# Performance work log

Hardware: AMD Instinct MI355X
Metric: run time of the kernel (lower is better)

The kernel has to match this reference:

```python
import jax, jax.numpy as jnp
import numpy as np

DWT_SCALE = 0.5   # per-tap Haar analysis scale (2D factor = 0.25)
IDWT_SCALE = 1.0  # per-tap Haar synthesis scale (exact inverse of 0.5 analysis)
CONV_PAD = 1      # (kernel_size - 1) // 2 for k = 3


def haar_dwt(x, s):
    # x: [B, C, H, W] -> [B, 4C, H/2, W/2], subband-major: [LL | LH | HL | HH]
    a = x[..., 0::2, 0::2]
    b = x[..., 0::2, 1::2]
    c = x[..., 1::2, 0::2]
    d = x[..., 1::2, 1::2]
    s2 = s * s
    ll = s2 * (a + b + c + d)
    lh = s2 * (a + b - c - d)
    hl = s2 * (a - b + c - d)
    hh = s2 * (a - b - c + d)
    return jnp.concatenate([ll, lh, hl, hh], axis=1)


def haar_idwt(y, t):
    # y: [B, 4C, H2, W2] -> [B, C, 2*H2, 2*W2]; exact inverse of haar_dwt when t*s == 0.5 per tap? (t=1, s=0.5 here)
    B, C4, H2, W2 = y.shape
    C = C4 // 4
    ll, lh, hl, hh = jnp.split(y, 4, axis=1)
    t2 = t * t
    a = t2 * (ll + lh + hl + hh)
    b = t2 * (ll + lh - hl - hh)
    c = t2 * (ll - lh + hl - hh)
    d = t2 * (ll - lh - hl + hh)
    top = jnp.stack([a, b], axis=-1).reshape(B, C, H2, 2 * W2)
    bot = jnp.stack([c, d], axis=-1).reshape(B, C, H2, 2 * W2)
    return jnp.stack([top, bot], axis=-2).reshape(B, C, 2 * H2, 2 * W2)


def conv2d(x, w, stride, pad):
    return jax.lax.conv_general_dilated(
        x, w, (stride, stride), [(pad, pad), (pad, pad)],
        dimension_numbers=('NCHW', 'OIHW', 'NCHW'))


def setup_inputs() -> dict:
    key = jax.random.key(0)
    ks = jax.random.split(key, 5)
    B, C, H, W, K, L = 4, 64, 192, 192, 3, 3
    x = jax.random.normal(ks[0], (B, C, H, W), dtype=jnp.float32)
    # kaiming_uniform_ with a=2.236: bound = sqrt(6 / ((1 + a^2) * fan_in))
    fan_in = 4 * C * K * K
    bound = float(np.sqrt(6.0 / ((1.0 + 2.236 ** 2) * fan_in)))
    inp = {'x': x}
    for i in range(L):
        inp[f'w{i}'] = jax.random.uniform(ks[1 + i], (4 * C, 4 * C, K, K), jnp.float32, -bound, bound)
    inp['bias'] = jnp.zeros((C,), jnp.float32)
    return inp


def reference(x, w0, w1, w2, bias):
    H, W = x.shape[-2:]
    weights = [w0, w1, w2]
    L = len(weights)
    pad_factor = 2 ** L
    pad_h = (-H) % pad_factor
    pad_w = (-W) % pad_factor
    xp = x
    if pad_h > 0 or pad_w > 0:
        xp = jnp.pad(x, ((0, 0), (0, 0), (0, pad_h), (0, pad_w)), mode='reflect')
    # decompose: DWT -> dense conv over stacked subbands; recurse on the conv'd LL band
    curr = xp
    highs = []
    for w in weights:
        d = haar_dwt(curr, DWT_SCALE)          # [B, 4C, H/2, W/2]
        y = conv2d(d, w, 1, CONV_PAD)          # [B, 4C_out, H/2, W/2]
        c_out = w.shape[0] // 4
        curr = y[:, :c_out]                    # LL -> next level
        highs.append(y[:, c_out:])             # LH, HL, HH kept for reconstruction
    # reconstruct bottom-up
    ll = curr
    for h in reversed(highs):
        ll = haar_idwt(jnp.concatenate([ll, h], axis=1), IDWT_SCALE)
    out = ll[..., :H, :W] + bias[None, :, None, None]
    return out
```

## Files before the change

### kernel.cpp

```cpp
#include <hip/hip_runtime.h>
#include <hip/hip_bf16.h>
#include <cstddef>


typedef __attribute__((ext_vector_type(8))) short short8;
typedef __attribute__((ext_vector_type(4))) float f32x4;
typedef __attribute__((ext_vector_type(4))) unsigned short u16x4;

static __device__ __forceinline__ unsigned short f2bf(float f) {
    __hip_bfloat16 h = __float2bfloat16(f);
    return *reinterpret_cast<unsigned short*>(&h);
}
static __device__ __forceinline__ float bf2f(unsigned short u) {
    return __uint_as_float(((unsigned int)u) << 16);
}

static __device__ __forceinline__ void gload_lds16(const short* g, short* l) {
    __builtin_amdgcn_global_load_lds(
        (const __attribute__((address_space(1))) void*)g,
        (__attribute__((address_space(3))) void*)l, 16, 0, 0);
}

__global__ __launch_bounds__(256) void mega_prep_kernel(
    const float* __restrict__ x,
    const float* __restrict__ wa, const float* __restrict__ wb,
    const float* __restrict__ wc,
    unsigned short* __restrict__ ta, unsigned short* __restrict__ tb,
    unsigned short* __restrict__ tc,
    unsigned short* __restrict__ p0, unsigned short* __restrict__ p1,
    unsigned short* __restrict__ p2)
{
    __shared__ float lds[4 * 64 * 17];
    const int bx = blockIdx.x;
    const int tid = threadIdx.x;
    if (bx < 864) {
        const int sel = bx / 288;
        const float* w = (sel == 0) ? wa : (sel == 1) ? wb : wc;
        unsigned short* wT = (sel == 0) ? ta : (sel == 1) ? tb : tc;
        int idx = (bx - sel * 288) * 256 + tid;
        int co = idx & 255;
        int g = (idx >> 8) & 3;
        int kb = (idx >> 10) & 7;
        int tap = idx >> 13;
        int cin0 = kb * 32 + g * 8;
        unsigned short tmp[8];
#pragma unroll
        for (int e = 0; e < 8; ++e)
            tmp[e] = f2bf(w[((size_t)co * 256 + cin0 + e) * 9 + tap]);
        *(short8*)(wT + (size_t)idx * 8) = *(const short8*)tmp;
        return;
    }
    if (bx < 1206) {
        constexpr int N0 = 49664, N1 = 25088, N2 = 12800;
        int idx = (bx - 864) * 256 + tid;
        unsigned short* base; int HP, WP, rel;
        if (idx < N0)           { base = p0; HP = 98; WP = 98; rel = idx; }
        else if (idx < N0 + N1) { base = p1; HP = 50; WP = 50; rel = idx - N0; }
        else                    { base = p2; HP = 26; WP = 26; rel = idx - N0 - N1; }
        int nb = 64 * WP + (HP - 2) * 64;
        int b = rel / nb, r = rel % nb;
        int row, kg, px;
        if (r < 64 * WP) {
            int rowSel = r / (32 * WP), rr = r % (32 * WP);
            kg = rr / WP; px = rr % WP; row = rowSel ? (HP - 1) : 0;
        } else {
            int r2 = r - 64 * WP;
            row = 1 + (r2 >> 6);
            int r3 = r2 & 63;
            kg = r3 >> 1; px = (r3 & 1) ? (WP - 1) : 0;
        }
        size_t o = (((size_t)(b * HP + row) * 32 + kg) * WP + px) * 8;
        short8 z = {};
        *(short8*)(base + o) = z;
        return;
    }
    const int bx2 = bx - 1206;
    const int j0 = (bx2 % 6) * 16;
    const int i  = (bx2 / 6) % 96;
    const int b  = bx2 / 576;
    const int j = tid & 15;
    const int c4 = tid >> 4;
#pragma unroll
    for (int it = 0; it < 4; ++it) {
        int c = c4 + it * 16;
        const float* p = x + ((size_t)(b * 64 + c) * 192 + 2 * i) * 192 + 2 * (j0 + j);
        float2 top = *(const float2*)p;
        float2 bot = *(const float2*)(p + 192);
        float a = top.x, bb = top.y, cc = bot.x, dd = bot.y;
        const float s2 = 0.25f;
        lds[(0 * 64 + c) * 17 + j] = s2 * (a + bb + cc + dd);
        lds[(1 * 64 + c) * 17 + j] = s2 * (a + bb - cc - dd);
        lds[(2 * 64 + c) * 17 + j] = s2 * (a - bb + cc - dd);
        lds[(3 * 64 + c) * 17 + j] = s2 * (a - bb - cc + dd);
    }
    __syncthreads();
#pragma unroll
    for (int it = 0; it < 2; ++it) {
        int idx = it * 256 + tid;
        int jj = idx & 15;
        int g = (idx >> 4) & 3;
        int kb = idx >> 6;
        int sub = kb >> 1;
        int c0 = (kb & 1) * 32 + g * 8;
        unsigned short tmp[8];
#pragma unroll
        for (int e = 0; e < 8; ++e)
            tmp[e] = f2bf(lds[(sub * 64 + c0 + e) * 17 + jj]);
        size_t o = ((((size_t)(b * 98 + 1 + i) * 8 + kb) * 4 + g) * 98 + 1 + j0 + jj) * 8;
        *(short8*)(p0 + o) = *(const short8*)tmp;
    }
}

template <int H2, int JB>
__global__ __launch_bounds__(256) void dwt_mid_kernel(
    const unsigned short* __restrict__ in, unsigned short* __restrict__ Xp)
{
    constexpr int W2 = H2, Wi = 2 * W2, WPn = W2 + 2, HPn = H2 + 2;
    constexpr int LS = JB + 1;
    __shared__ float lds[4 * 64 * LS];
    const int j0 = blockIdx.x * JB;
    const int i = blockIdx.y;
    const int b = blockIdx.z;
    const int tid = threadIdx.x;
    const int c = tid & 63;
    const int jq = tid >> 6;
#pragma unroll
    for (int it = 0; it < JB / 4; ++it) {
        int jl = jq + it * 4;
        int j = j0 + jl;
        const unsigned short* p = in + ((size_t)(b * 2 * H2 + 2 * i) * Wi + 2 * j) * 256 + c;
        float a  = bf2f(p[0]);
        float bb = bf2f(p[256]);
        float cc = bf2f(p[(size_t)Wi * 256]);
        float dd = bf2f(p[(size_t)Wi * 256 + 256]);
        const float s2 = 0.25f;
        lds[(0 * 64 + c) * LS + jl] = s2 * (a + bb + cc + dd);
        lds[(1 * 64 + c) * LS + jl] = s2 * (a + bb - cc - dd);
        lds[(2 * 64 + c) * LS + jl] = s2 * (a - bb + cc - dd);
        lds[(3 * 64 + c) * LS + jl] = s2 * (a - bb - cc + dd);
    }
    __syncthreads();
    constexpr int CH = 8 * 4 * JB;
#pragma unroll
    for (int it = 0; it < (CH + 255) / 256; ++it) {
        int idx = it * 256 + tid;
        if (idx < CH) {
            int jj = idx % JB;
            int g = (idx / JB) & 3;
            int kb = idx / (JB * 4);
            int sub = kb >> 1;
            int c0 = (kb & 1) * 32 + g * 8;
            unsigned short tmp[8];
#pragma unroll
            for (int e = 0; e < 8; ++e)
                tmp[e] = f2bf(lds[(sub * 64 + c0 + e) * LS + jj]);
            size_t o = ((((size_t)(b * HPn + 1 + i) * 8 + kb) * 4 + g) * WPn + 1 + j0 + jj) * 8;
            *(short8*)(Xp + o) = *(const short8*)tmp;
        }
    }
}

template <int HP, int WP, int PR, int PC, int XCHUNK>
__global__ __launch_bounds__(128) void conv_reg_kernel(
    const short* __restrict__ Xp, const short* __restrict__ Wt,
    unsigned short* __restrict__ Y)
{
    constexpr int WN = 2;
    constexpr int NPX = PR * PC;
    constexpr int MFR = 4;
    constexpr int NFR = NPX / (16 * WN);
    constexpr int RPF = 16 / PC;
    constexpr int BROWS = (NFR - 1) * RPF + 3;
    constexpr int H = HP - 2, W = WP - 2;
    constexpr int rowT = H / PR, colT = W / PC;
    constexpr int PH = PR + 2, PW = PC + 2;
    constexpr int RAW = PH * PW;
    constexpr int SLOTG = (RAW + 63) & ~63;
    constexpr int TI = 4 * SLOTG / 64;
    constexpr int TIW = TI / WN;
    constexpr size_t S_r = (size_t)256 * WP;
    constexpr size_t S_kb = (size_t)32 * WP;
    constexpr size_t S_g = (size_t)8 * WP;

    __shared__ __align__(16) short bufA[4 * SLOTG * 8];
    __shared__ __align__(16) short bufB[4 * SLOTG * 8];

    int bid = blockIdx.x;
    if (XCHUNK > 0) bid = (bid & 7) * XCHUNK + (bid >> 3);
    const int tx = bid % colT; bid /= colT;
    const int ty = bid % rowT; bid /= rowT;
    const int b = bid;
    const int gy0 = ty * PR;
    const int gx0 = tx * PC;
    const int cb = blockIdx.y * 64;

    const int lane = threadIdx.x & 63;
    const int wn = threadIdx.x >> 6;
    const int n15 = lane & 15, gq = lane >> 4;

    const size_t bBase = (size_t)(b * HP + gy0) * S_r + (size_t)gx0 * 8;

    size_t sSrc[TIW]; int sDst[TIW];
#pragma unroll
    for (int ti = 0; ti < TIW; ++ti) {
        int t = wn * TIW + ti;
        int d = t * 64 + lane;
        int g = d / SLOTG;
        int p = d - g * SLOTG;
        int prow = p / PW, pcol = p - prow * PW;
        sDst[ti] = d * 8;
        sSrc[ti] = (p < RAW)
            ? bBase + (size_t)prow * S_r + (size_t)g * S_g + (size_t)pcol * 8
            : bBase;
    }

    const short* aBase = Wt + (size_t)gq * 2048 + (size_t)(cb + n15) * 8;
    const int rB = wn * (PR / WN) + n15 / PC;
    const int cB = n15 % PC;
    const int bSlot = gq * SLOTG + rB * PW + cB;

    f32x4 acc[MFR][NFR] = {};
    short8 a[3][MFR];

    auto stage = [&](int kbv, short* dBuf) {
#pragma unroll
        for (int ti = 0; ti < TIW; ++ti)
            gload_lds16(Xp + sSrc[ti] + (size_t)kbv * S_kb, dBuf + sDst[ti]);
    };
    auto ldA = [&](int tap, int kbv, int m) -> short8 {
        return *(const short8*)(aBase + (size_t)tap * 65536
                                + (size_t)kbv * 8192 + m * 128);
    };

    stage(0, bufA);
#pragma unroll
    for (int s = 0; s < 3; ++s)
#pragma unroll
        for (int m = 0; m < MFR; ++m)
            a[s][m] = ldA(s, 0, m);
    asm volatile("s_waitcnt vmcnt(0)" ::: "memory");
    __builtin_amdgcn_sched_barrier(0);
    __builtin_amdgcn_s_barrier();

    auto kbBody = [&](int kb, const short* cur, short* nxt) {
        const int kbn = (kb < 7) ? kb + 1 : 7;
        stage(kbn, nxt);
        __builtin_amdgcn_sched_barrier(0);
        short8 Br[BROWS][3];
#pragma unroll
        for (int r = 0; r < BROWS; ++r)
#pragma unroll
            for (int kx = 0; kx < 3; ++kx)
                Br[r][kx] = *(const short8*)(cur + (bSlot + r * PW + kx) * 8);
#pragma unroll
        for (int s = 0; s < 9; ++s) {
            const int ky = s / 3, kx = s - 3 * (s / 3);
            const int rs = s % 3;
            __builtin_amdgcn_s_setprio(1);
#pragma unroll
            for (int m = 0; m < MFR; ++m)
#pragma unroll
                for (int n = 0; n < NFR; ++n)
                    acc[m][n] = __builtin_amdgcn_mfma_f32_16x16x32_bf16(
                        a[rs][m], Br[n * RPF + ky][kx], acc[m][n], 0, 0, 0);
            __builtin_amdgcn_s_setprio(0);
            const int ft = s + 3;
            const int ftap = (ft < 9) ? ft : ft - 9;
            const int fkb = (ft < 9) ? kb : kbn;
#pragma unroll
            for (int m = 0; m < MFR; ++m)
                a[rs][m] = ldA(ftap, fkb, m);
        }
        __builtin_amdgcn_sched_barrier(0);
        asm volatile("s_waitcnt vmcnt(36)" ::: "memory");
        __builtin_amdgcn_sched_barrier(0);
        __builtin_amdgcn_s_barrier();
    };

#pragma unroll 1
    for (int u = 0; u < 4; ++u) {
        kbBody(2 * u, bufA, bufB);
        kbBody(2 * u + 1, bufB, bufA);
    }
    asm volatile("s_waitcnt vmcnt(0)" ::: "memory");

#pragma unroll
    for (int m = 0; m < MFR; ++m)
#pragma unroll
        for (int n = 0; n < NFR; ++n) {
            int cout = cb + m * 16 + gq * 4;
            int row = wn * (PR / WN) + n * RPF + n15 / PC;
            int col = n15 % PC;
            unsigned short* op = Y + ((size_t)(b * H + gy0 + row) * W + gx0 + col) * 256 + cout;
            u16x4 sv;
#pragma unroll
            for (int q = 0; q < 4; ++q) sv[q] = f2bf(acc[m][n][q]);
            *(u16x4*)op = sv;
        }
}

__global__ __launch_bounds__(256) void idwt_fused_kernel(
    const unsigned short* __restrict__ y2, const unsigned short* __restrict__ y1,
    const unsigned short* __restrict__ y0h,
    const float* __restrict__ bias, float* __restrict__ out)
{
    __shared__ float lds[16 * 324];
    const int tt = blockIdx.x;
    const int tyi = tt / 12, txi = tt % 12;
    const int y0 = tyi * 8, x0 = txi * 8;
    const int cg = blockIdx.y;
    const int b = blockIdx.z;
    const int tid = threadIdx.x;

#pragma unroll
    for (int rep = 0; rep < 4; ++rep) {
        int idx = rep * 256 + tid;
        int c16 = idx & 15;
        int px = idx >> 4;
        int pi = px >> 3, pj = px & 7;
        int c = cg * 16 + c16;
        int pi96 = y0 + pi, pj96 = x0 + pj;
        int pi48 = pi96 >> 1, pj48 = pj96 >> 1;
        int pi24 = pi48 >> 1, pj24 = pj48 >> 1;
        const unsigned short* h2 = y2 + ((size_t)(b * 24 + pi24) * 24 + pj24) * 256;
        float l2   = bf2f(h2[c]);
        float l2lh = bf2f(h2[64 + c]);
        float l2hl = bf2f(h2[128 + c]);
        float l2hh = bf2f(h2[192 + c]);
        float s1 = 1.f - 2.f * (pi48 & 1), t1 = 1.f - 2.f * (pj48 & 1);
        float ll1v = l2 + s1 * l2lh + t1 * l2hl + (s1 * t1) * l2hh;
        const unsigned short* h1 = y1 + ((size_t)(b * 48 + pi48) * 48 + pj48) * 256;
        float l1lh = bf2f(h1[64 + c]);
        float l1hl = bf2f(h1[128 + c]);
        float l1hh = bf2f(h1[192 + c]);
        float s0 = 1.f - 2.f * (pi96 & 1), t0 = 1.f - 2.f * (pj96 & 1);
        float vll = ll1v + s0 * l1lh + t0 * l1hl + (s0 * t0) * l1hh;
        const unsigned short* hp = y0h + ((size_t)(b * 96 + pi96) * 96 + pj96) * 256;
        float vlh = bf2f(hp[64 + c]);
        float vhl = bf2f(hp[128 + c]);
        float vhh = bf2f(hp[192 + c]);
        float bv = bias[c];
        float a  = vll + vlh + vhl + vhh + bv;
        float b2 = vll + vlh - vhl - vhh + bv;
        float c2 = vll - vlh + vhl - vhh + bv;
        float d2 = vll - vlh - vhl + vhh + bv;
        float* l = lds + c16 * 324 + (2 * pi) * 20 + 2 * pj;
        l[0] = a; l[1] = b2;
        l[20] = c2; l[21] = d2;
    }
    __syncthreads();

    const int c16 = tid >> 4;
    const int yy = tid & 15;
    const float* l = lds + c16 * 324 + yy * 20;
    float* op = out + ((size_t)(b * 64 + cg * 16 + c16) * 192 + tyi * 16 + yy) * 192 + txi * 16;
#pragma unroll
    for (int q = 0; q < 4; ++q)
        *(f32x4*)(op + 4 * q) = *(const f32x4*)(l + 4 * q);
}

extern "C" void kernel_launch(void* const* d_in, const int* in_sizes, int n_in,
                              void* d_out, int out_size, void* d_ws, size_t ws_size,
                              hipStream_t stream)
{
    const float* x    = (const float*)d_in[0];
    const float* w0   = (const float*)d_in[1];
    const float* w1   = (const float*)d_in[2];
    const float* w2   = (const float*)d_in[3];
    const float* bias = (const float*)d_in[4];
    float* out = (float*)d_out;

    char* ws = (char*)d_ws;
    unsigned short* wT0 = (unsigned short*)(ws + 0);
    unsigned short* wT1 = (unsigned short*)(ws + 1179648);
    unsigned short* wT2 = (unsigned short*)(ws + 2359296);
    unsigned short* Xp0 = (unsigned short*)(ws + 3538944);
    unsigned short* Xp1 = (unsigned short*)(ws + 23207936);
    unsigned short* Xp2 = (unsigned short*)(ws + 28327936);
    unsigned short* y0 = (unsigned short*)(ws + 29712384);
    unsigned short* y1 = (unsigned short*)(ws + 48586752);
    unsigned short* y2 = (unsigned short*)(ws + 53305344);

    mega_prep_kernel<<<3510, 256, 0, stream>>>(x, w0, w1, w2, wT0, wT1, wT2,
                                               Xp0, Xp1, Xp2);

    conv_reg_kernel<98, 98, 4, 16, 72><<<dim3(576, 4), 128, 0, stream>>>(
        (const short*)Xp0, (const short*)wT0, y0);

    dwt_mid_kernel<48, 16><<<dim3(3, 48, 4), 256, 0, stream>>>(y0, Xp1);
    conv_reg_kernel<50, 50, 4, 16, 18><<<dim3(144, 4), 128, 0, stream>>>(
        (const short*)Xp1, (const short*)wT1, y1);

    dwt_mid_kernel<24, 12><<<dim3(2, 24, 4), 256, 0, stream>>>(y1, Xp2);
    conv_reg_kernel<26, 26, 4, 8, 9><<<dim3(72, 4), 128, 0, stream>>>(
        (const short*)Xp2, (const short*)wT2, y2);

    idwt_fused_kernel<<<dim3(144, 4, 4), 256, 0, stream>>>(y2, y1, y0, bias, out);
}
```

Baseline: 131.9 us.

## Switch conv kernels to 32x32x16 MFMA with square 8x8 pixel tiles

Replaces the 16x16x32 MFMA implicit-GEMM conv with a 32x32x16 MFMA variant. Each block now covers an 8x8 pixel tile, with each wave holding 32 pixels by 64 output channels in two 16-wide accumulators. This cuts the number of MFMA issues and B-fragment LDS reads per tap. The trade-offs are a different weight-fragment layout and a smaller 3-level grid (36 blocks), which loses the XCD chunking there and may underfill the GPU.

```diff
diff --git a/kernel.cpp b/kernel.cpp
--- a/kernel.cpp
+++ b/kernel.cpp
@@ -5,6 +5,7 @@
 
 typedef __attribute__((ext_vector_type(8))) short short8;
 typedef __attribute__((ext_vector_type(4))) float f32x4;
+typedef __attribute__((ext_vector_type(16))) float f32x16;
 typedef __attribute__((ext_vector_type(4))) unsigned short u16x4;
 
 static __device__ __forceinline__ unsigned short f2bf(float f) {
@@ -160,24 +161,17 @@
     }
 }
 
-template <int HP, int WP, int PR, int PC, int XCHUNK>
-__global__ __launch_bounds__(128) void conv_reg_kernel(
+template <int HP, int WP, int XCHUNK>
+__global__ __launch_bounds__(128) void conv32_kernel(
     const short* __restrict__ Xp, const short* __restrict__ Wt,
     unsigned short* __restrict__ Y)
 {
-    constexpr int WN = 2;
-    constexpr int NPX = PR * PC;
-    constexpr int MFR = 4;
-    constexpr int NFR = NPX / (16 * WN);
-    constexpr int RPF = 16 / PC;
-    constexpr int BROWS = (NFR - 1) * RPF + 3;
     constexpr int H = HP - 2, W = WP - 2;
-    constexpr int rowT = H / PR, colT = W / PC;
-    constexpr int PH = PR + 2, PW = PC + 2;
+    constexpr int rowT = H / 8, colT = W / 8;
+    constexpr int PH = 10, PW = 10;
     constexpr int RAW = PH * PW;
-    constexpr int SLOTG = (RAW + 63) & ~63;
-    constexpr int TI = 4 * SLOTG / 64;
-    constexpr int TIW = TI / WN;
+    constexpr int SLOTG = 128;
+    constexpr int TIW = 4;
     constexpr size_t S_r = (size_t)256 * WP;
     constexpr size_t S_kb = (size_t)32 * WP;
     constexpr size_t S_g = (size_t)8 * WP;
@@ -190,54 +184,57 @@
     const int tx = bid % colT; bid /= colT;
     const int ty = bid % rowT; bid /= rowT;
     const int b = bid;
-    const int gy0 = ty * PR;
-    const int gx0 = tx * PC;
+    const int gy0 = ty * 8;
+    const int gx0 = tx * 8;
     const int cb = blockIdx.y * 64;
 
     const int lane = threadIdx.x & 63;
     const int wn = threadIdx.x >> 6;
-    const int n15 = lane & 15, gq = lane >> 4;
+    const int l31 = lane & 31;
+    const int kg2 = lane >> 5;
 
     const size_t bBase = (size_t)(b * HP + gy0) * S_r + (size_t)gx0 * 8;
 
     size_t sSrc[TIW]; int sDst[TIW];
 #pragma unroll
     for (int ti = 0; ti < TIW; ++ti) {
-        int t = wn * TIW + ti;
-        int d = t * 64 + lane;
-        int g = d / SLOTG;
-        int p = d - g * SLOTG;
-        int prow = p / PW, pcol = p - prow * PW;
+        int d = (wn * TIW + ti) * 64 + lane;
+        int g = d >> 7;
+        int slot = d & 127;
+        int prow = slot / PW, pcol = slot % PW;
         sDst[ti] = d * 8;
-        sSrc[ti] = (p < RAW)
+        sSrc[ti] = (slot < RAW)
             ? bBase + (size_t)prow * S_r + (size_t)g * S_g + (size_t)pcol * 8
             : bBase;
     }
 
-    const short* aBase = Wt + (size_t)gq * 2048 + (size_t)(cb + n15) * 8;
-    const int rB = wn * (PR / WN) + n15 / PC;
-    const int cB = n15 % PC;
-    const int bSlot = gq * SLOTG + rB * PW + cB;
-
-    f32x4 acc[MFR][NFR] = {};
-    short8 a[3][MFR];
+    const short* aBase = Wt + (size_t)(cb + l31) * 8;
+    const int prow = wn * 4 + (l31 >> 3);
+    const int pcol = l31 & 7;
+    const int bSlot = prow * PW + pcol;
+
+    f32x16 acc[2] = {};
+    short8 a[3][2][2];
 
     auto stage = [&](int kbv, short* dBuf) {
 #pragma unroll
         for (int ti = 0; ti < TIW; ++ti)
             gload_lds16(Xp + sSrc[ti] + (size_t)kbv * S_kb, dBuf + sDst[ti]);
     };
-    auto ldA = [&](int tap, int kbv, int m) -> short8 {
+    auto ldA = [&](int tap, int kbv, int h, int m) -> short8 {
         return *(const short8*)(aBase + (size_t)tap * 65536
-                                + (size_t)kbv * 8192 + m * 128);
+                                + (size_t)kbv * 8192
+                                + (size_t)(h * 2 + kg2) * 2048 + m * 256);
     };
 
     stage(0, bufA);
 #pragma unroll
     for (int s = 0; s < 3; ++s)
 #pragma unroll
-        for (int m = 0; m < MFR; ++m)
-            a[s][m] = ldA(s, 0, m);
+        for (int h = 0; h < 2; ++h)
+#pragma unroll
+            for (int m = 0; m < 2; ++m)
+                a[s][h][m] = ldA(s, 0, h, m);
     asm volatile("s_waitcnt vmcnt(0)" ::: "memory");
     __builtin_amdgcn_sched_barrier(0);
     __builtin_amdgcn_s_barrier();
@@ -246,30 +243,35 @@
         const int kbn = (kb < 7) ? kb + 1 : 7;
         stage(kbn, nxt);
         __builtin_amdgcn_sched_barrier(0);
-        short8 Br[BROWS][3];
-#pragma unroll
-        for (int r = 0; r < BROWS; ++r)
-#pragma unroll
-            for (int kx = 0; kx < 3; ++kx)
-                Br[r][kx] = *(const short8*)(cur + (bSlot + r * PW + kx) * 8);
+        short8 Br[2][3][3];
+#pragma unroll
+        for (int h = 0; h < 2; ++h)
+#pragma unroll
+            for (int ky = 0; ky < 3; ++ky)
+#pragma unroll
+                for (int kx = 0; kx < 3; ++kx)
+                    Br[h][ky][kx] = *(const short8*)(cur
+                        + ((h * 2 + kg2) * SLOTG + bSlot + ky * PW + kx) * 8);
 #pragma unroll
         for (int s = 0; s < 9; ++s) {
             const int ky = s / 3, kx = s - 3 * (s / 3);
             const int rs = s % 3;
             __builtin_amdgcn_s_setprio(1);
 #pragma unroll
-            for (int m = 0; m < MFR; ++m)
-#pragma unroll
-                for (int n = 0; n < NFR; ++n)
-                    acc[m][n] = __builtin_amdgcn_mfma_f32_16x16x32_bf16(
-                        a[rs][m], Br[n * RPF + ky][kx], acc[m][n], 0, 0, 0);
+            for (int h = 0; h < 2; ++h)
+#pragma unroll
+                for (int m = 0; m < 2; ++m)
+                    acc[m] = __builtin_amdgcn_mfma_f32_32x32x16_bf16(
+                        a[rs][h][m], Br[h][ky][kx], acc[m], 0, 0, 0);
             __builtin_amdgcn_s_setprio(0);
             const int ft = s + 3;
             const int ftap = (ft < 9) ? ft : ft - 9;
             const int fkb = (ft < 9) ? kb : kbn;
 #pragma unroll
-            for (int m = 0; m < MFR; ++m)
-                a[rs][m] = ldA(ftap, fkb, m);
+            for (int h = 0; h < 2; ++h)
+#pragma unroll
+                for (int m = 0; m < 2; ++m)
+                    a[rs][h][m] = ldA(ftap, fkb, h, m);
         }
         __builtin_amdgcn_sched_barrier(0);
         asm volatile("s_waitcnt vmcnt(36)" ::: "memory");
@@ -285,16 +287,15 @@
     asm volatile("s_waitcnt vmcnt(0)" ::: "memory");
 
 #pragma unroll
-    for (int m = 0; m < MFR; ++m)
-#pragma unroll
-        for (int n = 0; n < NFR; ++n) {
-            int cout = cb + m * 16 + gq * 4;
-            int row = wn * (PR / WN) + n * RPF + n15 / PC;
-            int col = n15 % PC;
-            unsigned short* op = Y + ((size_t)(b * H + gy0 + row) * W + gx0 + col) * 256 + cout;
+    for (int m = 0; m < 2; ++m)
+#pragma unroll
+        for (int q = 0; q < 4; ++q) {
+            int cout = cb + m * 32 + 8 * q + 4 * kg2;
+            unsigned short* op = Y + ((size_t)(b * H + gy0 + prow) * W
+                                      + gx0 + pcol) * 256 + cout;
             u16x4 sv;
 #pragma unroll
-            for (int q = 0; q < 4; ++q) sv[q] = f2bf(acc[m][n][q]);
+            for (int t = 0; t < 4; ++t) sv[t] = f2bf(acc[m][4 * q + t]);
             *(u16x4*)op = sv;
         }
 }
@@ -384,15 +385,15 @@
     mega_prep_kernel<<<3510, 256, 0, stream>>>(x, w0, w1, w2, wT0, wT1, wT2,
                                                Xp0, Xp1, Xp2);
 
-    conv_reg_kernel<98, 98, 4, 16, 72><<<dim3(576, 4), 128, 0, stream>>>(
+    conv32_kernel<98, 98, 72><<<dim3(576, 4), 128, 0, stream>>>(
         (const short*)Xp0, (const short*)wT0, y0);
 
     dwt_mid_kernel<48, 16><<<dim3(3, 48, 4), 256, 0, stream>>>(y0, Xp1);
-    conv_reg_kernel<50, 50, 4, 16, 18><<<dim3(144, 4), 128, 0, stream>>>(
+    conv32_kernel<50, 50, 18><<<dim3(144, 4), 128, 0, stream>>>(
         (const short*)Xp1, (const short*)wT1, y1);
 
     dwt_mid_kernel<24, 12><<<dim3(2, 24, 4), 256, 0, stream>>>(y1, Xp2);
-    conv_reg_kernel<26, 26, 4, 8, 9><<<dim3(72, 4), 128, 0, stream>>>(
+    conv32_kernel<26, 26, 0><<<dim3(36, 4), 128, 0, stream>>>(
         (const short*)Xp2, (const short*)wT2, y2);
 
     idwt_fused_kernel<<<dim3(144, 4, 4), 256, 0, stream>>>(y2, y1, y0, bias, out);
```

Measured after the change: 136.8 us. 1.04x slower.
